# Kernel tuning notes

Measured on AMD Instinct MI355X. Metric: run time of the kernel, lower is better.

## Reference

```python
import jax, jax.numpy as jnp
import numpy as np

B, S, D_MODEL, H = 4, 2048, 2048, 16
HEAD_DIM = D_MODEL // H  # 128
SCALE = HEAD_DIM ** -0.5


def setup_inputs() -> dict:
    key = jax.random.key(0)
    ks = jax.random.split(key, 9)
    std = D_MODEL ** -0.5
    inp = {
        "x": jax.random.normal(ks[0], (B, S, D_MODEL), dtype=jnp.float32),
        "mask": jnp.ones((B, 1, S, S), dtype=jnp.int32),
        "Wq": jax.random.normal(ks[1], (D_MODEL, D_MODEL), dtype=jnp.float32) * std,
        "bq": jnp.zeros((D_MODEL,), dtype=jnp.float32),
        "Wk": jax.random.normal(ks[2], (D_MODEL, D_MODEL), dtype=jnp.float32) * std,
        "bk": jnp.zeros((D_MODEL,), dtype=jnp.float32),
        "Wv": jax.random.normal(ks[3], (D_MODEL, D_MODEL), dtype=jnp.float32) * std,
        "bv": jnp.zeros((D_MODEL,), dtype=jnp.float32),
        "Wo": jax.random.normal(ks[4], (D_MODEL, D_MODEL), dtype=jnp.float32) * std,
        "bo": jnp.zeros((D_MODEL,), dtype=jnp.float32),
    }
    return inp


def reference(x, mask, Wq, bq, Wk, bk, Wv, bv, Wo, bo):
    b, s, d = x.shape
    # projections: [B,S,D] -> [B,S,H,HEAD_DIM] -> [B,H,S,HEAD_DIM]
    def proj(W, bias):
        y = jnp.einsum("bsd,de->bse", x, W) + bias
        return y.reshape(b, s, H, HEAD_DIM).transpose(0, 2, 1, 3)

    q = proj(Wq, bq)
    k = proj(Wk, bk)
    v = proj(Wv, bv)

    scores = jnp.einsum("bhqd,bhkd->bhqk", q, k) * SCALE  # [B,H,S,S]
    scores = jnp.where(mask == 0, -jnp.inf, scores)
    attn = jax.nn.softmax(scores, axis=-1)
    out = jnp.einsum("bhqk,bhkd->bhqd", attn, v)  # [B,H,S,HEAD_DIM]
    out = out.transpose(0, 2, 1, 3).reshape(b, s, d)
    return jnp.einsum("bsd,de->bse", out, Wo) + bo
```

## Files before the change

kernel.cpp:

```cpp
#include <hip/hip_runtime.h>


typedef __bf16 bf16;
typedef __bf16 bf16x4 __attribute__((ext_vector_type(4)));
typedef __bf16 bf16x8 __attribute__((ext_vector_type(8)));
typedef float  f32x4  __attribute__((ext_vector_type(4)));

#define S_TOK 2048
#define DMODEL 2048
#define NHEAD 16
#define HDIM 128
#define BH_STRIDE ((size_t)S_TOK * HDIM)
#define KT32 (DMODEL / 32)
#define TILE_ELEMS 4096
#define QSCALE (0.08838834764831845f * 1.4426950408889634f)

__device__ __forceinline__ void load_lds16(const void* g, void* l) {
  __builtin_amdgcn_global_load_lds((const __attribute__((address_space(1))) void*)g,
                                   (__attribute__((address_space(3))) void*)l,
                                   16, 0, 0);
}


__global__ __launch_bounds__(256) void pack_a(const float* __restrict__ X,
                                              bf16* __restrict__ dst) {
  __shared__ bf16 lds[128 * 32];
  const int t = threadIdx.x;
  const int kt = blockIdx.x, mt = blockIdx.y;
  const int k0 = kt * 32, m0 = mt * 128;
#pragma unroll
  for (int p = 0; p < 4; ++p) {
    int r = p * 32 + (t >> 3);
    int c = (t & 7) * 4;
    float4 v = *(const float4*)(X + (size_t)(m0 + r) * DMODEL + k0 + c);
    lds[r * 32 + c + 0] = (bf16)v.x;
    lds[r * 32 + c + 1] = (bf16)v.y;
    lds[r * 32 + c + 2] = (bf16)v.z;
    lds[r * 32 + c + 3] = (bf16)v.w;
  }
  __syncthreads();
  bf16* out = dst + ((size_t)mt * 64 + kt) * TILE_ELEMS;
#pragma unroll
  for (int u = 0; u < 2; ++u) {
    int c = t * 2 + u;
    int f = c >> 6, lane = c & 63;
    int l16 = lane & 15, q = lane >> 4;
    bf16x8 v;
#pragma unroll
    for (int e = 0; e < 8; ++e)
      v[e] = lds[(f * 16 + l16) * 32 + q * 8 + e];
    *(bf16x8*)(out + (size_t)c * 8) = v;
  }
}

__global__ __launch_bounds__(256) void pack_w(const float* __restrict__ W,
                                              bf16* __restrict__ dst) {
  __shared__ bf16 lds[32 * 128];
  const int t = threadIdx.x;
  const int kt = blockIdx.x, nt = blockIdx.y;
  const int k0 = kt * 32, n0 = nt * 128;
#pragma unroll
  for (int p = 0; p < 4; ++p) {
    int kl = (t >> 5) + p * 8;
    int nl = (t & 31) * 4;
    float4 v = *(const float4*)(W + (size_t)(k0 + kl) * DMODEL + n0 + nl);
    lds[kl * 128 + nl + 0] = (bf16)v.x;
    lds[kl * 128 + nl + 1] = (bf16)v.y;
    lds[kl * 128 + nl + 2] = (bf16)v.z;
    lds[kl * 128 + nl + 3] = (bf16)v.w;
  }
  __syncthreads();
  bf16* out = dst + ((size_t)nt * KT32 + kt) * TILE_ELEMS;
#pragma unroll
  for (int u = 0; u < 2; ++u) {
    int c = t * 2 + u;
    int i_g = c >> 6, quad = (c >> 4) & 3, l16 = c & 15;
    bf16x8 v;
#pragma unroll
    for (int e = 0; e < 8; ++e)
      v[e] = lds[(quad * 8 + e) * 128 + i_g * 16 + l16];
    *(bf16x8*)(out + (size_t)c * 8) = v;
  }
}

__global__ __launch_bounds__(256) void v_chunk(const bf16* __restrict__ vb,
                                               bf16* __restrict__ vc) {
  __shared__ alignas(16) bf16 t[64 * 128];
  const int tid = threadIdx.x;
  const int s0 = blockIdx.x * 64;
  const size_t bhoff = (size_t)blockIdx.y * BH_STRIDE;
  const bf16* src = vb + bhoff + (size_t)s0 * HDIM;
#pragma unroll
  for (int r = 0; r < 4; ++r) {
    int c = r * 256 + tid;
    *(bf16x8*)(t + (size_t)c * 8) = *(const bf16x8*)(src + (size_t)(c >> 4) * HDIM + (c & 15) * 8);
  }
  __syncthreads();
  bf16* dst = vc + bhoff + (size_t)(s0 >> 3) * (HDIM * 8);
#pragma unroll
  for (int r = 0; r < 4; ++r) {
    int c = r * 256 + tid;
    int scl = c >> 7, d = c & 127;
    bf16x8 v;
#pragma unroll
    for (int e = 0; e < 8; ++e) v[e] = t[(size_t)(scl * 8 + e) * HDIM + d];
    *(bf16x8*)(dst + (size_t)scl * (HDIM * 8) + d * 8) = v;
  }
}

__global__ __launch_bounds__(512, 2) void gemm_qkv(
    const bf16* __restrict__ apack, const bf16* __restrict__ wpack,
    const float* __restrict__ bq, const float* __restrict__ bk, const float* __restrict__ bv,
    bf16* __restrict__ qc, bf16* __restrict__ kc_, bf16* __restrict__ vb) {
  __shared__ alignas(16) bf16 sBuf[3 * 16384];
  const int tid = threadIdx.x, wave = tid >> 6, lane = tid & 63;
  const int quad = lane >> 4, l16 = lane & 15;
  const int wm = wave >> 2, wn = wave & 3;

  const int lin = blockIdx.x;
  const int swz = (lin & 7) * 96 + (lin >> 3);
  const int mt = swz & 31, nt = swz >> 5;
  const int m0 = mt * 256, n0 = nt * 256;

  const bf16* srcA0 = apack + (size_t)(mt * 2 + 0) * KT32 * TILE_ELEMS + (size_t)tid * 8;
  const bf16* srcA1 = apack + (size_t)(mt * 2 + 1) * KT32 * TILE_ELEMS + (size_t)tid * 8;
  const bf16* srcB0 = wpack + (size_t)(nt * 2 + 0) * KT32 * TILE_ELEMS + (size_t)tid * 8;
  const bf16* srcB1 = wpack + (size_t)(nt * 2 + 1) * KT32 * TILE_ELEMS + (size_t)tid * 8;

  f32x4 acc[8][4];
  const f32x4 zero = {0.f, 0.f, 0.f, 0.f};
#pragma unroll
  for (int i = 0; i < 8; ++i)
#pragma unroll
    for (int j = 0; j < 4; ++j) acc[i][j] = zero;

  bf16* sD = sBuf + (size_t)tid * 8;

  load_lds16(srcA0, sD);
  load_lds16(srcA1, sD + 4096);
  load_lds16(srcB0, sD + 8192);
  load_lds16(srcB1, sD + 12288);
  load_lds16(srcA0 + TILE_ELEMS, sD + 16384);
  load_lds16(srcA1 + TILE_ELEMS, sD + 16384 + 4096);
  load_lds16(srcB0 + TILE_ELEMS, sD + 16384 + 8192);
  load_lds16(srcB1 + TILE_ELEMS, sD + 16384 + 12288);

  const bf16* ldsA = sBuf + (size_t)wm * 4096 + (size_t)lane * 8;
  const bf16* ldsB = sBuf + 8192 + (size_t)(wn >> 1) * 4096
                   + (size_t)((wn & 1) * 4) * 512 + (size_t)lane * 8;

  int buf = 0, nbuf = 2;
#pragma unroll 1
  for (int t = 0; t < KT32; ++t) {
    if (t == KT32 - 1) { asm volatile("s_waitcnt vmcnt(0)" ::: "memory"); }
    else               { asm volatile("s_waitcnt vmcnt(4)" ::: "memory"); }
    __builtin_amdgcn_s_barrier();
    asm volatile("" ::: "memory");

    const bf16* bA = ldsA + buf * 16384;
    const bf16* bB = ldsB + buf * 16384;

    bf16x8 bfr[4], afr[4];
#pragma unroll
    for (int j = 0; j < 4; ++j) bfr[j] = *(const bf16x8*)(bB + (size_t)j * 512);
#pragma unroll
    for (int i = 0; i < 4; ++i) afr[i] = *(const bf16x8*)(bA + (size_t)i * 512);
    if (t < KT32 - 2) {
      bf16* d = sD + nbuf * 16384;
      load_lds16(srcA0 + (size_t)(t + 2) * TILE_ELEMS, d);
      load_lds16(srcA1 + (size_t)(t + 2) * TILE_ELEMS, d + 4096);
    }
    __builtin_amdgcn_s_setprio(1);
#pragma unroll
    for (int i = 0; i < 4; ++i)
#pragma unroll
      for (int j = 0; j < 4; ++j)
        acc[i][j] = __builtin_amdgcn_mfma_f32_16x16x32_bf16(bfr[j], afr[i], acc[i][j], 0, 0, 0);
    __builtin_amdgcn_s_setprio(0);

#pragma unroll
    for (int i = 0; i < 4; ++i) afr[i] = *(const bf16x8*)(bA + (size_t)(4 + i) * 512);
    if (t < KT32 - 2) {
      bf16* d = sD + nbuf * 16384;
      load_lds16(srcB0 + (size_t)(t + 2) * TILE_ELEMS, d + 8192);
      load_lds16(srcB1 + (size_t)(t + 2) * TILE_ELEMS, d + 12288);
    }
    __builtin_amdgcn_s_setprio(1);
#pragma unroll
    for (int i = 0; i < 4; ++i)
#pragma unroll
      for (int j = 0; j < 4; ++j)
        acc[4 + i][j] = __builtin_amdgcn_mfma_f32_16x16x32_bf16(bfr[j], afr[i], acc[4 + i][j], 0, 0, 0);
    __builtin_amdgcn_s_setprio(0);

    buf  = (buf  == 2) ? 0 : buf  + 1;
    nbuf = (nbuf == 2) ? 0 : nbuf + 1;
  }

  const float* bias; bf16* dst; int chunked; float oscale;
  if (n0 < 2048)      { bias = bq; dst = qc;  chunked = 1; oscale = QSCALE; }
  else if (n0 < 4096) { bias = bk; dst = kc_; chunked = 1; oscale = 1.0f; }
  else                { bias = bv; dst = vb;  chunked = 0; oscale = 1.0f; }
  const int nb = n0 & 2047;
  const int rw = wm * 128, cw = wn * 64;
#pragma unroll
  for (int i = 0; i < 8; ++i) {
    int m = m0 + rw + i * 16 + l16;
    int b = m >> 11, s = m & 2047;
#pragma unroll
    for (int j = 0; j < 4; ++j) {
      int n = nb + cw + j * 16 + quad * 4;
      int h = n >> 7, d = n & 127;
      bf16x4 v;
#pragma unroll
      for (int r = 0; r < 4; ++r) v[r] = (bf16)((acc[i][j][r] + bias[n + r]) * oscale);
      size_t bhoff = (size_t)(b * NHEAD + h) * BH_STRIDE;
      if (chunked)
        *(bf16x4*)(dst + bhoff + (size_t)(d >> 3) * (S_TOK * 8) + (size_t)s * 8 + (d & 7)) = v;
      else
        *(bf16x4*)(dst + bhoff + (size_t)s * HDIM + d) = v;
    }
  }
}

__device__ __forceinline__ void gemm_core_lds(const bf16* __restrict__ A,
                                              const bf16* __restrict__ wpanel,
                                              int m0, bf16* sA, f32x4 acc[4][4]) {
  const int tid = threadIdx.x;
  const int wave = tid >> 6, lane = tid & 63;
  const int quad = lane >> 4, l16 = lane & 15;
  const int rw = (wave >> 1) * 64;

  const f32x4 zero = {0.f, 0.f, 0.f, 0.f};
#pragma unroll
  for (int i = 0; i < 4; ++i)
#pragma unroll
    for (int j = 0; j < 4; ++j) acc[i][j] = zero;

  const int kb0 = tid >> 7;
  const int row = tid & 127;
  const bf16* a0 = A + (size_t)(m0 + row) * DMODEL + kb0 * 8;
  const bf16* a1 = a0 + 16;
  const bf16* wb = wpanel + (size_t)(wave & 1) * 4 * 512 + (size_t)lane * 8;

  load_lds16(a0, sA + tid * 8); load_lds16(a1, sA + (256 + tid) * 8);
  a0 += 32; a1 += 32;
  bf16x8 wfc[4], wfn[4];
#pragma unroll
  for (int j = 0; j < 4; ++j)
    wfc[j] = *(const bf16x8*)(wb + (size_t)j * 512);

#pragma unroll 2
  for (int kt = 0; kt < KT32; ++kt) {
    __syncthreads();
    const int cur = kt & 1, nxt = cur ^ 1;
    if (kt + 1 < KT32) {
      load_lds16(a0, sA + (nxt * 512 + tid) * 8);
      load_lds16(a1, sA + (nxt * 512 + 256 + tid) * 8);
      a0 += 32; a1 += 32;
      const bf16* wn = wb + (size_t)(kt + 1) * TILE_ELEMS;
#pragma unroll
      for (int j = 0; j < 4; ++j)
        wfn[j] = *(const bf16x8*)(wn + (size_t)j * 512);
    }
    const bf16* sAc = sA + cur * 4096;
    bf16x8 xf[4];
#pragma unroll
    for (int i = 0; i < 4; ++i)
      xf[i] = *(const bf16x8*)(sAc + ((size_t)quad * 128 + rw + i * 16 + l16) * 8);
#pragma unroll
    for (int i = 0; i < 4; ++i)
#pragma unroll
      for (int j = 0; j < 4; ++j)
        acc[i][j] = __builtin_amdgcn_mfma_f32_16x16x32_bf16(wfc[j], xf[i], acc[i][j], 0, 0, 0);
#pragma unroll
    for (int j = 0; j < 4; ++j) wfc[j] = wfn[j];
  }
}

__global__ __launch_bounds__(256) void gemm_out(
    const bf16* __restrict__ A, const bf16* __restrict__ wpack,
    const float* __restrict__ bo, float* __restrict__ out) {
  __shared__ alignas(16) bf16 sA[2 * 4096];
  const int m0 = blockIdx.x * 128, n0 = blockIdx.y * 128;
  f32x4 acc[4][4];
  gemm_core_lds(A, wpack + (size_t)blockIdx.y * KT32 * TILE_ELEMS, m0, sA, acc);

  const int tid = threadIdx.x, wave = tid >> 6, lane = tid & 63;
  const int quad = lane >> 4, l16 = lane & 15;
  const int rw = (wave >> 1) * 64, cw = (wave & 1) * 64;
#pragma unroll
  for (int i = 0; i < 4; ++i) {
    int m = m0 + rw + i * 16 + l16;
#pragma unroll
    for (int j = 0; j < 4; ++j) {
      int n = n0 + cw + j * 16 + quad * 4;
      f32x4 v = acc[i][j];
#pragma unroll
      for (int r = 0; r < 4; ++r) v[r] += bo[n + r];
      *(f32x4*)(out + (size_t)m * DMODEL + n) = v;
    }
  }
}

__global__ __launch_bounds__(256) void flash_kernel(
    const bf16* __restrict__ qc, const bf16* __restrict__ kcg,
    const bf16* __restrict__ vcg, bf16* __restrict__ ob) {
  __shared__ alignas(16) bf16 sK[16 * 64 * 8];
  __shared__ alignas(16) bf16 sV[8 * 128 * 8];
  __shared__ alignas(16) bf16 sP[8 * 1024];

  const int tid = threadIdx.x, wave = tid >> 6, lane = tid & 63;
  const int quad = lane >> 4, l16 = lane & 15;
  const int bh = blockIdx.y;
  const int q0 = blockIdx.x * 128;

  const bf16* Qg = qc  + (size_t)bh * BH_STRIDE;
  const bf16* Kg = kcg + (size_t)bh * BH_STRIDE;
  const bf16* Vg = vcg + (size_t)bh * BH_STRIDE;

  bf16x8 qf[2][4];
#pragma unroll
  for (int qs = 0; qs < 2; ++qs)
#pragma unroll
    for (int ks = 0; ks < 4; ++ks)
      qf[qs][ks] = *(const bf16x8*)(Qg + (size_t)(ks * 4 + quad) * (S_TOK * 8)
                                       + (size_t)(q0 + wave * 32 + qs * 16 + l16) * 8);

  bf16* sPw = sP + wave * 2048;

  float m_i[2] = {-1e30f, -1e30f}, l_i[2] = {0.f, 0.f};
  f32x4 o[2][8];
  const f32x4 zero = {0.f, 0.f, 0.f, 0.f};
#pragma unroll
  for (int qs = 0; qs < 2; ++qs)
#pragma unroll
    for (int dt = 0; dt < 8; ++dt) o[qs][dt] = zero;

  for (int kv = 0; kv < S_TOK; kv += 64) {
    __syncthreads();
#pragma unroll
    for (int r = 0; r < 4; ++r) {
      int c = r * 256 + tid;
      load_lds16(Kg + (size_t)(c >> 6) * (S_TOK * 8) + (size_t)(kv + (c & 63)) * 8,
                 sK + (size_t)c * 8);
    }
#pragma unroll
    for (int r = 0; r < 4; ++r) {
      int c = r * 256 + tid;
      load_lds16(Vg + (size_t)((kv >> 3) + (c >> 7)) * (HDIM * 8) + (size_t)(c & 127) * 8,
                 sV + (size_t)c * 8);
    }
    __syncthreads();

    f32x4 sc[2][4];
    __builtin_amdgcn_s_setprio(1);
#pragma unroll
    for (int i = 0; i < 4; ++i) {
      sc[0][i] = zero; sc[1][i] = zero;
#pragma unroll
      for (int ks = 0; ks < 4; ++ks) {
        bf16x8 kf = *(const bf16x8*)(sK + ((size_t)(ks * 4 + quad) * 64 + i * 16 + l16) * 8);
        sc[0][i] = __builtin_amdgcn_mfma_f32_16x16x32_bf16(kf, qf[0][ks], sc[0][i], 0, 0, 0);
        sc[1][i] = __builtin_amdgcn_mfma_f32_16x16x32_bf16(kf, qf[1][ks], sc[1][i], 0, 0, 0);
      }
    }
    __builtin_amdgcn_s_setprio(0);

    float tmax[2];
#pragma unroll
    for (int qs = 0; qs < 2; ++qs) {
      f32x4 tm = sc[qs][0];
#pragma unroll
      for (int i = 1; i < 4; ++i)
#pragma unroll
        for (int r = 0; r < 4; ++r) tm[r] = fmaxf(tm[r], sc[qs][i][r]);
      float mx = fmaxf(fmaxf(tm[0], tm[1]), fmaxf(tm[2], tm[3]));
      mx = fmaxf(mx, __shfl_xor(mx, 16));
      mx = fmaxf(mx, __shfl_xor(mx, 32));
      tmax[qs] = mx;
    }

    bool ok = (tmax[0] - m_i[0] <= 8.0f) && (tmax[1] - m_i[1] <= 8.0f);
    if (!__all(ok)) {
#pragma unroll
      for (int qs = 0; qs < 2; ++qs) {
        float mnew = fmaxf(m_i[qs], tmax[qs]);
        float alpha = __builtin_amdgcn_exp2f(m_i[qs] - mnew);
        m_i[qs] = mnew;
        l_i[qs] *= alpha;
#pragma unroll
        for (int dt = 0; dt < 8; ++dt) o[qs][dt] = o[qs][dt] * alpha;
      }
    }

#pragma unroll
    for (int qs = 0; qs < 2; ++qs) {
      f32x4 rsv = zero;
      bf16x4 pv[4];
#pragma unroll
      for (int i = 0; i < 4; ++i)
#pragma unroll
        for (int r = 0; r < 4; ++r) {
          float pe = __builtin_amdgcn_exp2f(sc[qs][i][r] - m_i[qs]);
          rsv[r] += pe;
          pv[i][r] = (bf16)pe;
        }
      float rs = (rsv[0] + rsv[1]) + (rsv[2] + rsv[3]);
      rs += __shfl_xor(rs, 16);
      rs += __shfl_xor(rs, 32);
      l_i[qs] += rs;
#pragma unroll
      for (int i = 0; i < 4; ++i)
        *(bf16x4*)(sPw + (size_t)qs * 1024
                   + (size_t)(i * 2 + (quad >> 1)) * 128 + l16 * 8 + (quad & 1) * 4) = pv[i];
    }

    bf16x8 pf[2][2];
#pragma unroll
    for (int qs = 0; qs < 2; ++qs) {
      pf[qs][0] = *(const bf16x8*)(sPw + (size_t)qs * 1024 + (size_t)(quad * 16 + l16) * 8);
      pf[qs][1] = *(const bf16x8*)(sPw + (size_t)qs * 1024 + (size_t)((4 + quad) * 16 + l16) * 8);
    }
    __builtin_amdgcn_s_setprio(1);
#pragma unroll
    for (int dt = 0; dt < 8; ++dt) {
      bf16x8 vf0 = *(const bf16x8*)(sV + ((size_t)quad * 128 + dt * 16 + l16) * 8);
      bf16x8 vf1 = *(const bf16x8*)(sV + ((size_t)(4 + quad) * 128 + dt * 16 + l16) * 8);
      o[0][dt] = __builtin_amdgcn_mfma_f32_16x16x32_bf16(vf0, pf[0][0], o[0][dt], 0, 0, 0);
      o[0][dt] = __builtin_amdgcn_mfma_f32_16x16x32_bf16(vf1, pf[0][1], o[0][dt], 0, 0, 0);
      o[1][dt] = __builtin_amdgcn_mfma_f32_16x16x32_bf16(vf0, pf[1][0], o[1][dt], 0, 0, 0);
      o[1][dt] = __builtin_amdgcn_mfma_f32_16x16x32_bf16(vf1, pf[1][1], o[1][dt], 0, 0, 0);
    }
    __builtin_amdgcn_s_setprio(0);
  }

  int b = bh >> 4, h = bh & 15;
#pragma unroll
  for (int qs = 0; qs < 2; ++qs) {
    float inv = 1.0f / l_i[qs];
    int s = q0 + wave * 32 + qs * 16 + l16;
    bf16* orow = ob + ((size_t)(b * S_TOK + s) * DMODEL + h * HDIM);
#pragma unroll
    for (int dt = 0; dt < 8; ++dt) {
      bf16x4 v;
#pragma unroll
      for (int r = 0; r < 4; ++r) v[r] = (bf16)(o[qs][dt][r] * inv);
      *(bf16x4*)(orow + dt * 16 + quad * 4) = v;
    }
  }
}


extern "C" void kernel_launch(void* const* d_in, const int* in_sizes, int n_in,
                              void* d_out, int out_size, void* d_ws, size_t ws_size,
                              hipStream_t stream) {
  const float* x  = (const float*)d_in[0];
  const float* Wq = (const float*)d_in[2];
  const float* bq = (const float*)d_in[3];
  const float* Wk = (const float*)d_in[4];
  const float* bk = (const float*)d_in[5];
  const float* Wv = (const float*)d_in[6];
  const float* bv = (const float*)d_in[7];
  const float* Wo = (const float*)d_in[8];
  const float* bo = (const float*)d_in[9];
  float* out = (float*)d_out;

  const size_t M = 4 * (size_t)S_TOK;
  const size_t SZ_TOK = M * DMODEL * 2;
  const size_t SZ_WMAT = (size_t)16 * KT32 * TILE_ELEMS * 2;

  char* p = (char*)d_ws;
  bf16* ap  = (bf16*)p; p += SZ_TOK;
  bf16* wp  = (bf16*)p; p += 3 * SZ_WMAT;
  bf16* wop = (bf16*)p; p += SZ_WMAT;
  bf16* qc  = (bf16*)p; p += SZ_TOK;
  bf16* kc  = (bf16*)p; p += SZ_TOK;
  bf16* vb  = (bf16*)p; p += SZ_TOK;
  bf16* vc  = (bf16*)p; p += SZ_TOK;
  bf16* ob  = ap;

  pack_a<<<dim3(64, 64), 256, 0, stream>>>(x, ap);
  pack_w<<<dim3(KT32, 16), 256, 0, stream>>>(Wq, wp);
  pack_w<<<dim3(KT32, 16), 256, 0, stream>>>(Wk, wp + SZ_WMAT / 2);
  pack_w<<<dim3(KT32, 16), 256, 0, stream>>>(Wv, wp + SZ_WMAT);
  pack_w<<<dim3(KT32, 16), 256, 0, stream>>>(Wo, wop);

  gemm_qkv<<<dim3(768), dim3(512), 0, stream>>>(ap, wp, bq, bk, bv, qc, kc, vb);
  v_chunk<<<dim3(32, 64), 256, 0, stream>>>(vb, vc);
  flash_kernel<<<dim3(16, 64), 256, 0, stream>>>(qc, kc, vc, ob);
  gemm_out<<<dim3(64, 16), 256, 0, stream>>>(ob, wop, bo, out);
}
```

Before: 751.6 us.

## Process flash attention KV tile in 16-key chunks with deferred row-sum reduction

Restructures the per-tile flash attention loop so scores are computed and softmaxed in four 16-key chunks, each pair immediately fed into the PV MFMAs. This cuts live score registers and halves the P scratch in LDS. The launch bounds now request 4 blocks per CU. The per-row sum is kept per lane and reduced across lanes only once at the end, and the max reduction runs only when a rescale is needed. The trade-off is more frequent rescale checks and smaller MFMA batches between LDS round trips, which may reduce instruction-level overlap.

```diff
diff --git a/kernel.cpp b/kernel.cpp
--- a/kernel.cpp
+++ b/kernel.cpp
@@ -303,12 +303,12 @@
   }
 }
 
-__global__ __launch_bounds__(256) void flash_kernel(
+__global__ __launch_bounds__(256, 4) void flash_kernel(
     const bf16* __restrict__ qc, const bf16* __restrict__ kcg,
     const bf16* __restrict__ vcg, bf16* __restrict__ ob) {
   __shared__ alignas(16) bf16 sK[16 * 64 * 8];
   __shared__ alignas(16) bf16 sV[8 * 128 * 8];
-  __shared__ alignas(16) bf16 sP[8 * 1024];
+  __shared__ alignas(16) bf16 sP[4 * 1024];
 
   const int tid = threadIdx.x, wave = tid >> 6, lane = tid & 63;
   const int quad = lane >> 4, l16 = lane & 15;
@@ -327,9 +327,10 @@
       qf[qs][ks] = *(const bf16x8*)(Qg + (size_t)(ks * 4 + quad) * (S_TOK * 8)
                                        + (size_t)(q0 + wave * 32 + qs * 16 + l16) * 8);
 
-  bf16* sPw = sP + wave * 2048;
-
-  float m_i[2] = {-1e30f, -1e30f}, l_i[2] = {0.f, 0.f};
+  bf16* sPw = sP + wave * 1024;
+
+  float m_i[2] = {-1e30f, -1e30f};
+  float l_i[2] = {0.f, 0.f};
   f32x4 o[2][8];
   const f32x4 zero = {0.f, 0.f, 0.f, 0.f};
 #pragma unroll
@@ -337,6 +338,7 @@
 #pragma unroll
     for (int dt = 0; dt < 8; ++dt) o[qs][dt] = zero;
 
+#pragma unroll 1
   for (int kv = 0; kv < S_TOK; kv += 64) {
     __syncthreads();
 #pragma unroll
@@ -353,92 +355,80 @@
     }
     __syncthreads();
 
-    f32x4 sc[2][4];
-    __builtin_amdgcn_s_setprio(1);
-#pragma unroll
-    for (int i = 0; i < 4; ++i) {
-      sc[0][i] = zero; sc[1][i] = zero;
-#pragma unroll
-      for (int ks = 0; ks < 4; ++ks) {
-        bf16x8 kf = *(const bf16x8*)(sK + ((size_t)(ks * 4 + quad) * 64 + i * 16 + l16) * 8);
-        sc[0][i] = __builtin_amdgcn_mfma_f32_16x16x32_bf16(kf, qf[0][ks], sc[0][i], 0, 0, 0);
-        sc[1][i] = __builtin_amdgcn_mfma_f32_16x16x32_bf16(kf, qf[1][ks], sc[1][i], 0, 0, 0);
+#pragma unroll
+    for (int pp = 0; pp < 2; ++pp) {
+#pragma unroll
+      for (int sub = 0; sub < 2; ++sub) {
+        const int ch = pp * 2 + sub;
+        f32x4 sc0 = zero, sc1 = zero;
+        __builtin_amdgcn_s_setprio(1);
+#pragma unroll
+        for (int ks = 0; ks < 4; ++ks) {
+          bf16x8 kf = *(const bf16x8*)(sK + ((size_t)(ks * 4 + quad) * 64 + ch * 16 + l16) * 8);
+          sc0 = __builtin_amdgcn_mfma_f32_16x16x32_bf16(kf, qf[0][ks], sc0, 0, 0, 0);
+          sc1 = __builtin_amdgcn_mfma_f32_16x16x32_bf16(kf, qf[1][ks], sc1, 0, 0, 0);
+        }
+        __builtin_amdgcn_s_setprio(0);
+
+        float t0 = fmaxf(fmaxf(sc0[0], sc0[1]), fmaxf(sc0[2], sc0[3]));
+        float t1 = fmaxf(fmaxf(sc1[0], sc1[1]), fmaxf(sc1[2], sc1[3]));
+        bool ok = (t0 - m_i[0] <= 8.0f) && (t1 - m_i[1] <= 8.0f);
+        if (!__all(ok)) {
+          float r0 = fmaxf(t0, __shfl_xor(t0, 16)); r0 = fmaxf(r0, __shfl_xor(r0, 32));
+          float r1 = fmaxf(t1, __shfl_xor(t1, 16)); r1 = fmaxf(r1, __shfl_xor(r1, 32));
+          float m0n = fmaxf(m_i[0], r0), a0 = __builtin_amdgcn_exp2f(m_i[0] - m0n);
+          float m1n = fmaxf(m_i[1], r1), a1 = __builtin_amdgcn_exp2f(m_i[1] - m1n);
+          m_i[0] = m0n; m_i[1] = m1n;
+          l_i[0] *= a0; l_i[1] *= a1;
+#pragma unroll
+          for (int dt = 0; dt < 8; ++dt) { o[0][dt] = o[0][dt] * a0; o[1][dt] = o[1][dt] * a1; }
+        }
+
+        bf16x4 pv0, pv1;
+        float s00, s01, s10, s11;
+        {
+          float p0 = __builtin_amdgcn_exp2f(sc0[0] - m_i[0]);
+          float p1 = __builtin_amdgcn_exp2f(sc0[1] - m_i[0]);
+          float p2 = __builtin_amdgcn_exp2f(sc0[2] - m_i[0]);
+          float p3 = __builtin_amdgcn_exp2f(sc0[3] - m_i[0]);
+          pv0[0] = (bf16)p0; pv0[1] = (bf16)p1; pv0[2] = (bf16)p2; pv0[3] = (bf16)p3;
+          s00 = p0 + p1; s01 = p2 + p3;
+        }
+        {
+          float p0 = __builtin_amdgcn_exp2f(sc1[0] - m_i[1]);
+          float p1 = __builtin_amdgcn_exp2f(sc1[1] - m_i[1]);
+          float p2 = __builtin_amdgcn_exp2f(sc1[2] - m_i[1]);
+          float p3 = __builtin_amdgcn_exp2f(sc1[3] - m_i[1]);
+          pv1[0] = (bf16)p0; pv1[1] = (bf16)p1; pv1[2] = (bf16)p2; pv1[3] = (bf16)p3;
+          s10 = p0 + p1; s11 = p2 + p3;
+        }
+        l_i[0] += s00 + s01;
+        l_i[1] += s10 + s11;
+        const int prow = (sub * 2 + (quad >> 1)) * 128 + l16 * 8 + (quad & 1) * 4;
+        *(bf16x4*)(sPw + prow) = pv0;
+        *(bf16x4*)(sPw + 512 + prow) = pv1;
       }
-    }
-    __builtin_amdgcn_s_setprio(0);
-
-    float tmax[2];
-#pragma unroll
-    for (int qs = 0; qs < 2; ++qs) {
-      f32x4 tm = sc[qs][0];
-#pragma unroll
-      for (int i = 1; i < 4; ++i)
-#pragma unroll
-        for (int r = 0; r < 4; ++r) tm[r] = fmaxf(tm[r], sc[qs][i][r]);
-      float mx = fmaxf(fmaxf(tm[0], tm[1]), fmaxf(tm[2], tm[3]));
-      mx = fmaxf(mx, __shfl_xor(mx, 16));
-      mx = fmaxf(mx, __shfl_xor(mx, 32));
-      tmax[qs] = mx;
-    }
-
-    bool ok = (tmax[0] - m_i[0] <= 8.0f) && (tmax[1] - m_i[1] <= 8.0f);
-    if (!__all(ok)) {
-#pragma unroll
-      for (int qs = 0; qs < 2; ++qs) {
-        float mnew = fmaxf(m_i[qs], tmax[qs]);
-        float alpha = __builtin_amdgcn_exp2f(m_i[qs] - mnew);
-        m_i[qs] = mnew;
-        l_i[qs] *= alpha;
-#pragma unroll
-        for (int dt = 0; dt < 8; ++dt) o[qs][dt] = o[qs][dt] * alpha;
+
+      bf16x8 pf0 = *(const bf16x8*)(sPw + (size_t)(quad * 128 + l16 * 8));
+      bf16x8 pf1 = *(const bf16x8*)(sPw + 512 + (size_t)(quad * 128 + l16 * 8));
+      __builtin_amdgcn_s_setprio(1);
+#pragma unroll
+      for (int dt = 0; dt < 8; ++dt) {
+        bf16x8 vf = *(const bf16x8*)(sV + ((size_t)(pp * 4 + quad) * 128 + dt * 16 + l16) * 8);
+        o[0][dt] = __builtin_amdgcn_mfma_f32_16x16x32_bf16(vf, pf0, o[0][dt], 0, 0, 0);
+        o[1][dt] = __builtin_amdgcn_mfma_f32_16x16x32_bf16(vf, pf1, o[1][dt], 0, 0, 0);
       }
-    }
-
-#pragma unroll
-    for (int qs = 0; qs < 2; ++qs) {
-      f32x4 rsv = zero;
-      bf16x4 pv[4];
-#pragma unroll
-      for (int i = 0; i < 4; ++i)
-#pragma unroll
-        for (int r = 0; r < 4; ++r) {
-          float pe = __builtin_amdgcn_exp2f(sc[qs][i][r] - m_i[qs]);
-          rsv[r] += pe;
-          pv[i][r] = (bf16)pe;
-        }
-      float rs = (rsv[0] + rsv[1]) + (rsv[2] + rsv[3]);
-      rs += __shfl_xor(rs, 16);
-      rs += __shfl_xor(rs, 32);
-      l_i[qs] += rs;
-#pragma unroll
-      for (int i = 0; i < 4; ++i)
-        *(bf16x4*)(sPw + (size_t)qs * 1024
-                   + (size_t)(i * 2 + (quad >> 1)) * 128 + l16 * 8 + (quad & 1) * 4) = pv[i];
-    }
-
-    bf16x8 pf[2][2];
-#pragma unroll
-    for (int qs = 0; qs < 2; ++qs) {
-      pf[qs][0] = *(const bf16x8*)(sPw + (size_t)qs * 1024 + (size_t)(quad * 16 + l16) * 8);
-      pf[qs][1] = *(const bf16x8*)(sPw + (size_t)qs * 1024 + (size_t)((4 + quad) * 16 + l16) * 8);
-    }
-    __builtin_amdgcn_s_setprio(1);
-#pragma unroll
-    for (int dt = 0; dt < 8; ++dt) {
-      bf16x8 vf0 = *(const bf16x8*)(sV + ((size_t)quad * 128 + dt * 16 + l16) * 8);
-      bf16x8 vf1 = *(const bf16x8*)(sV + ((size_t)(4 + quad) * 128 + dt * 16 + l16) * 8);
-      o[0][dt] = __builtin_amdgcn_mfma_f32_16x16x32_bf16(vf0, pf[0][0], o[0][dt], 0, 0, 0);
-      o[0][dt] = __builtin_amdgcn_mfma_f32_16x16x32_bf16(vf1, pf[0][1], o[0][dt], 0, 0, 0);
-      o[1][dt] = __builtin_amdgcn_mfma_f32_16x16x32_bf16(vf0, pf[1][0], o[1][dt], 0, 0, 0);
-      o[1][dt] = __builtin_amdgcn_mfma_f32_16x16x32_bf16(vf1, pf[1][1], o[1][dt], 0, 0, 0);
-    }
-    __builtin_amdgcn_s_setprio(0);
+      __builtin_amdgcn_s_setprio(0);
+    }
   }
 
   int b = bh >> 4, h = bh & 15;
 #pragma unroll
   for (int qs = 0; qs < 2; ++qs) {
-    float inv = 1.0f / l_i[qs];
+    float l = l_i[qs];
+    l += __shfl_xor(l, 16);
+    l += __shfl_xor(l, 32);
+    float inv = 1.0f / l;
     int s = q0 + wave * 32 + qs * 16 + l16;
     bf16* orow = ob + ((size_t)(b * S_TOK + s) * DMODEL + h * HDIM);
 #pragma unroll
```

After: 780.8 us. 1.04x slower.
